# Kernel tuning notes

Hardware: AMD Instinct MI355X
Metric: run time of the kernel (lower is better)

## Reference

```python
import jax, jax.numpy as jnp
import numpy as np

EPS = 1e-5

def mesh_conv(x, gemm, w, b):
    # x: [B, C, E] edge features; gemm: [B, E, 4] int neighbor edge ids
    B, C, E = x.shape
    self_idx = jnp.broadcast_to(jnp.arange(E, dtype=gemm.dtype)[None, :, None], (B, E, 1))
    G = jnp.concatenate([self_idx, gemm], axis=2) + 1          # [B, E, 5], 0 = zero-pad slot
    xp = jnp.concatenate([jnp.zeros((B, C, 1), x.dtype), x], axis=2)  # [B, C, E+1]
    # f[b,c,e,k] = xp[b,c,G[b,e,k]]
    f = jax.vmap(lambda xb, gb: xb[:, gb])(xp, G)              # [B, C, E, 5]
    f0 = f[..., 0]
    x1 = f[..., 1] + f[..., 3]
    x2 = f[..., 2] + f[..., 4]
    x3 = jnp.abs(f[..., 1] - f[..., 3])
    x4 = jnp.abs(f[..., 2] - f[..., 4])
    Gm = jnp.stack([f0, x1, x2, x3, x4], axis=-1)              # [B, C, E, 5]
    # Conv2d kernel (1,5) over the 5 symmetric features
    out = jnp.einsum('bces,ocs->boe', Gm, w) + b[None, :, None]
    return out

def instance_norm(x):
    # InstanceNorm2d (affine=False): normalize per (b, c) over edge dim
    mean = jnp.mean(x, axis=2, keepdims=True)
    var = jnp.var(x, axis=2, keepdims=True)
    return (x - mean) * jax.lax.rsqrt(var + EPS)

def setup_inputs() -> dict:
    key = jax.random.key(0)
    ks = jax.random.split(key, 6)
    B, Cin, Cout, E = 2, 64, 128, 100000
    fe = jax.random.normal(ks[0], (B, Cin, E), dtype=jnp.float32)
    gemm = jax.random.randint(ks[1], (B, E, 4), 0, E, dtype=jnp.int32)
    w1 = jax.random.normal(ks[2], (Cout, Cin, 5), dtype=jnp.float32) * 0.05
    b1 = jax.random.normal(ks[3], (Cout,), dtype=jnp.float32) * 0.05
    w2 = jax.random.normal(ks[4], (Cout, Cout, 5), dtype=jnp.float32) * 0.05
    b2 = jax.random.normal(ks[5], (Cout,), dtype=jnp.float32) * 0.05
    return {"fe": fe, "gemm": gemm, "w1": w1, "b1": b1, "w2": w2, "b2": b2}

def reference(fe, gemm, w1, b1, w2, b2):
    x1 = jax.nn.relu(instance_norm(mesh_conv(fe, gemm, w1, b1)))
    x2 = instance_norm(mesh_conv(x1, gemm, w2, b2))
    x2 = jax.nn.relu(x2 + x1)
    return x2  # [B, Cout, E]; pool=0 so before_pool is None
```

## Files before the change

### kernel.cpp

```cpp
#include <hip/hip_runtime.h>
#include <hip/hip_bf16.h>

typedef unsigned short u16;
typedef __attribute__((ext_vector_type(4))) unsigned short u16x4;
typedef __attribute__((ext_vector_type(8))) unsigned short u16x8;
typedef __attribute__((ext_vector_type(8))) short s16x8;
typedef __attribute__((ext_vector_type(4))) float f32x4;

__device__ __forceinline__ float bf2f(u16 u){
  union { unsigned int i; float f; } v; v.i = ((unsigned int)u) << 16; return v.f;
}
__device__ __forceinline__ u16 f2bf(float f){
  union { float f; unsigned int i; } v; v.f = f;
  unsigned int r = v.i + 0x7fffu + ((v.i >> 16) & 1u);
  return (u16)(r >> 16);
}
__device__ __forceinline__ u16 f2bfh(float f){
  __hip_bfloat16 h = __float2bfloat16(f);
  return *reinterpret_cast<u16*>(&h);
}

__global__ __launch_bounds__(256) void prep_w(
    const float* __restrict__ src, u16* __restrict__ dst, int cout, int cin)
{
  const int n  = cout * cin * 5;
  const int KT = (cin * 5) / 32;
  const int i = blockIdx.x * 256 + threadIdx.x;
  if (i >= n) return;
  const int ii   = i & 7;
  const int lane = (i >> 3) & 63;
  const int kt   = (i >> 9) % KT;
  const int wv   = i / (KT * 512);
  const int o = wv * 16 + (lane & 15);
  const int k = kt * 32 + (lane >> 4) * 8 + ii;
  const int s = k / cin;
  const int c = k - s * cin;
  dst[i] = f2bf(src[(o * cin + c) * 5 + s]);
}

__global__ __launch_bounds__(256) void transpose64(
    const float* __restrict__ x, u16* __restrict__ xT, int E)
{
  __shared__ u16 tile[64][66];
  const int b   = blockIdx.z;
  const int e0  = blockIdx.x * 64;
  const int col = threadIdx.x & 63;
  const int r   = threadIdx.x >> 6;
  const int e   = e0 + col;
  #pragma unroll
  for (int k = 0; k < 16; k++) {
    const int c = r * 16 + k;
    float v = 0.f;
    if (e < E) v = x[((size_t)b * 64 + c) * (size_t)E + e];
    tile[c][col] = f2bf(v);
  }
  __syncthreads();
  const int e_l  = threadIdx.x >> 2;
  const int part = threadIdx.x & 3;
  const int eg   = e0 + e_l;
  if (eg < E) {
    u16* dst = xT + ((size_t)b * E + eg) * 64 + part * 16;
    #pragma unroll
    for (int h = 0; h < 2; h++) {
      u16x8 v;
      #pragma unroll
      for (int cc = 0; cc < 8; cc++) v[cc] = tile[part * 16 + h * 8 + cc][e_l];
      *(u16x8*)(dst + h * 8) = v;
    }
  }
}

__global__ __launch_bounds__(512, 6) void conv1_mfma(
    const u16* __restrict__ xT, const int* __restrict__ gidx,
    const u16* __restrict__ Wp, const float* __restrict__ bias,
    u16* __restrict__ y1b, float2* __restrict__ partials, int E, int nbx)
{
  constexpr int CIN = 64, EPB = 64, SUB = 8, KT = 10;
  constexpr int NT  = EPB / 16;
  __shared__ __align__(16) u16 F[5 * EPB * CIN];

  const int b  = blockIdx.z;
  const int bx = blockIdx.x;
  const int t  = threadIdx.x;
  const int e_l = t / SUB;
  const int sub = t % SUB;
  const int lane = t & 63, wv = t >> 6;
  const int lr = lane & 15, quad = lane >> 4;
  const size_t e_raw = (size_t)bx * EPB + e_l;
  const int e = (int)(e_raw < (size_t)E ? e_raw : (size_t)(E - 1));

  int rows[5];
  {
    const int4 g = *(const int4*)(gidx + ((size_t)b * E + e) * 4);
    rows[0] = e; rows[1] = g.x; rows[2] = g.y; rows[3] = g.z; rows[4] = g.w;
  }
  const u16* base = xT + (size_t)b * E * CIN + sub * 8;
  const u16* wbase = Wp + ((size_t)wv * KT * 64 + lane) * 8;

  u16x8 raw[5];
  #pragma unroll
  for (int j = 0; j < 5; j++)
    raw[j] = *(const u16x8*)(base + (size_t)rows[j] * CIN);
  __builtin_amdgcn_sched_barrier(0);

  {
    const int pc = (sub ^ (e_l & 7)) * 8;
    u16x8 o1, o2, o3, o4;
    #pragma unroll
    for (int c = 0; c < 8; c++) {
      const float a1 = bf2f(raw[1][c]), a2 = bf2f(raw[2][c]);
      const float a3 = bf2f(raw[3][c]), a4 = bf2f(raw[4][c]);
      o1[c] = f2bfh(a1 + a3);
      o2[c] = f2bfh(a2 + a4);
      o3[c] = f2bfh(fabsf(a1 - a3));
      o4[c] = f2bfh(fabsf(a2 - a4));
    }
    *(u16x8*)&F[(0 * EPB + e_l) * CIN + pc] = raw[0];
    *(u16x8*)&F[(1 * EPB + e_l) * CIN + pc] = o1;
    *(u16x8*)&F[(2 * EPB + e_l) * CIN + pc] = o2;
    *(u16x8*)&F[(3 * EPB + e_l) * CIN + pc] = o3;
    *(u16x8*)&F[(4 * EPB + e_l) * CIN + pc] = o4;
  }
  __syncthreads();

  f32x4 acc[NT];
  #pragma unroll
  for (int j = 0; j < NT; j++) acc[j] = (f32x4){0.f, 0.f, 0.f, 0.f};
  #pragma unroll
  for (int kt = 0; kt < KT; kt++) {
    const int s  = kt >> 1, cb = (kt & 1) * 32;
    const int chk = ((cb >> 3) + quad) ^ (lr & 7);
    const s16x8 a0 = *(const s16x8*)(wbase + kt * 512);
    #pragma unroll
    for (int j = 0; j < NT; j++) {
      const s16x8 bj = *(const s16x8*)&F[(s * EPB + j * 16 + lr) * CIN + chk * 8];
      acc[j] = __builtin_amdgcn_mfma_f32_16x16x32_bf16(bj, a0, acc[j], 0, 0, 0);
    }
  }

  const int ch = wv * 16 + lr;
  const float bv = bias[ch];
  float s = 0.f, s2 = 0.f;
  #pragma unroll
  for (int j = 0; j < NT; j++) {
    #pragma unroll
    for (int r = 0; r < 4; r++) {
      const int el = j * 16 + quad * 4 + r;
      const size_t eg = (size_t)bx * EPB + el;
      if (eg < (size_t)E) {
        const float v = acc[j][r] + bv;
        y1b[((size_t)b * E + eg) * 128 + ch] = f2bfh(v);
        s += v; s2 += v * v;
      }
    }
  }
  s  += __shfl_xor(s, 16);  s  += __shfl_xor(s, 32);
  s2 += __shfl_xor(s2, 16); s2 += __shfl_xor(s2, 32);
  if (lane < 16)
    partials[(size_t)(b * 128 + ch) * nbx + bx] = make_float2(s, s2);
}

__global__ __launch_bounds__(512, 6) void conv2_mfma(
    const u16* __restrict__ x1b, const int* __restrict__ gidx,
    const u16* __restrict__ Wp, const float* __restrict__ bias,
    const float2* __restrict__ stats1,
    u16* __restrict__ y2b, float2* __restrict__ partials, int E, int nbx)
{
  constexpr int CIN = 128, EPB = 32, SUB = 16, KT = 20;
  constexpr int NT  = EPB / 16;
  __shared__ __align__(16) u16 F[5 * EPB * CIN];

  const int b  = blockIdx.z;
  const int bx = blockIdx.x;
  const int t  = threadIdx.x;
  const int e_l = t / SUB;
  const int sub = t % SUB;
  const int lane = t & 63, wv = t >> 6;
  const int lr = lane & 15, quad = lane >> 4;
  const size_t e_raw = (size_t)bx * EPB + e_l;
  const int e = (int)(e_raw < (size_t)E ? e_raw : (size_t)(E - 1));

  int rows[5];
  {
    const int4 g = *(const int4*)(gidx + ((size_t)b * E + e) * 4);
    rows[0] = e; rows[1] = g.x; rows[2] = g.y; rows[3] = g.z; rows[4] = g.w;
  }
  const u16* base = x1b + (size_t)b * E * 128 + sub * 8;
  const u16* wbase = Wp + ((size_t)wv * KT * 64 + lane) * 8;

  u16x8 raw[5];
  #pragma unroll
  for (int j = 0; j < 5; j++)
    raw[j] = *(const u16x8*)(base + (size_t)rows[j] * 128);
  f32x4 st[4];
  {
    const float* sp = (const float*)(stats1 + b * 128 + sub * 8);
    #pragma unroll
    for (int q = 0; q < 4; q++) st[q] = *(const f32x4*)(sp + q * 4);
  }
  __builtin_amdgcn_sched_barrier(0);

  {
    const int pc = (sub ^ (e_l & 7)) * 8;
    u16x8 o0, o1, o2, o3, o4;
    #pragma unroll
    for (int c = 0; c < 8; c++) {
      const float nm = st[c >> 1][(c & 1) * 2];
      const float rr = st[c >> 1][(c & 1) * 2 + 1];
      float x[5];
      #pragma unroll
      for (int j = 0; j < 5; j++) {
        float v = fmaf(bf2f(raw[j][c]), rr, nm);
        x[j] = v < 0.f ? 0.f : v;
      }
      o0[c] = f2bfh(x[0]);
      o1[c] = f2bfh(x[1] + x[3]);
      o2[c] = f2bfh(x[2] + x[4]);
      o3[c] = f2bfh(fabsf(x[1] - x[3]));
      o4[c] = f2bfh(fabsf(x[2] - x[4]));
    }
    *(u16x8*)&F[(0 * EPB + e_l) * CIN + pc] = o0;
    *(u16x8*)&F[(1 * EPB + e_l) * CIN + pc] = o1;
    *(u16x8*)&F[(2 * EPB + e_l) * CIN + pc] = o2;
    *(u16x8*)&F[(3 * EPB + e_l) * CIN + pc] = o3;
    *(u16x8*)&F[(4 * EPB + e_l) * CIN + pc] = o4;
  }
  __syncthreads();

  f32x4 acc[NT];
  #pragma unroll
  for (int j = 0; j < NT; j++) acc[j] = (f32x4){0.f, 0.f, 0.f, 0.f};
  #pragma unroll
  for (int kt = 0; kt < KT; kt++) {
    const int s  = kt >> 2, cb = (kt & 3) * 32;
    const int chk = ((cb >> 3) + quad) ^ (lr & 7);
    const s16x8 a0 = *(const s16x8*)(wbase + kt * 512);
    #pragma unroll
    for (int j = 0; j < NT; j++) {
      const s16x8 bj = *(const s16x8*)&F[(s * EPB + j * 16 + lr) * CIN + chk * 8];
      acc[j] = __builtin_amdgcn_mfma_f32_16x16x32_bf16(a0, bj, acc[j], 0, 0, 0);
    }
  }

  const size_t ybase = (size_t)b * 128;
  const int m0 = wv * 16 + quad * 4;
  const float4 bs = *(const float4*)(bias + m0);
  #pragma unroll
  for (int r = 0; r < 4; r++) {
    const int m = m0 + r;
    const float bv = ((const float*)&bs)[r];
    float s = 0.f, s2 = 0.f;
    #pragma unroll
    for (int j = 0; j < NT; j++) {
      const size_t eg = (size_t)bx * EPB + j * 16 + lr;
      if (eg < (size_t)E) {
        const float v = acc[j][r] + bv;
        y2b[(ybase + m) * E + eg] = f2bfh(v);
        s += v; s2 += v * v;
      }
    }
    #pragma unroll
    for (int mk = 1; mk < 16; mk <<= 1) {
      s  += __shfl_xor(s,  mk);
      s2 += __shfl_xor(s2, mk);
    }
    if (lr == 0)
      partials[(size_t)(b * 128 + m) * nbx + bx] = make_float2(s, s2);
  }
}

__global__ __launch_bounds__(256) void stats_finalize(
    const float2* __restrict__ partials, float2* __restrict__ stats,
    int nbx, int E)
{
  const int row = blockIdx.x;
  const float2* p = partials + (size_t)row * nbx;
  float s = 0.f, s2 = 0.f;
  for (int i = threadIdx.x; i < nbx; i += 256) {
    const float2 v = p[i];
    s += v.x; s2 += v.y;
  }
  #pragma unroll
  for (int off = 32; off > 0; off >>= 1) {
    s  += __shfl_down(s, off);
    s2 += __shfl_down(s2, off);
  }
  __shared__ float rs[4], rs2[4];
  const int wv = threadIdx.x >> 6;
  if ((threadIdx.x & 63) == 0) { rs[wv] = s; rs2[wv] = s2; }
  __syncthreads();
  if (threadIdx.x == 0) {
    s  = rs[0] + rs[1] + rs[2] + rs[3];
    s2 = rs2[0] + rs2[1] + rs2[2] + rs2[3];
    const float mean = s / E;
    const float var  = s2 / E - mean * mean;
    const float rstd = rsqrtf(var + 1e-5f);
    stats[row] = make_float2(-mean * rstd, rstd);
  }
}

__global__ __launch_bounds__(256) void final_k(
    const u16* __restrict__ y2b, const u16* __restrict__ y1b,
    const float2* __restrict__ st1, const float2* __restrict__ st2,
    float* __restrict__ out, int E)
{
  __shared__ float tile[32][65];
  const int b  = blockIdx.z;
  const int o0 = blockIdx.y * 32;
  const int e0 = blockIdx.x * 64;
  const int t  = threadIdx.x;

  {
    const int e_l  = t >> 2;
    const int part = t & 3;
    const int eg   = e0 + e_l;
    if (eg < E) {
      const u16* src = y1b + ((size_t)b * E + eg) * 128 + o0 + part * 8;
      const u16x8 v = *(const u16x8*)src;
      #pragma unroll
      for (int i = 0; i < 8; i++) {
        const float2 s1 = st1[b * 128 + o0 + part * 8 + i];
        float x = fmaf(bf2f(v[i]), s1.y, s1.x);
        tile[part * 8 + i][e_l] = x < 0.f ? 0.f : x;
      }
    }
  }
  __syncthreads();

  {
    const int col = t & 63;
    const int r   = t >> 6;
    const int eg  = e0 + col;
    if (eg < E) {
      #pragma unroll
      for (int k = 0; k < 8; k++) {
        const int o = o0 + r * 8 + k;
        const float2 s2 = st2[b * 128 + o];
        const size_t idx = ((size_t)b * 128 + o) * E + eg;
        float v = fmaf(bf2f(y2b[idx]), s2.y, s2.x) + tile[r * 8 + k][col];
        v = v < 0.f ? 0.f : v;
        __builtin_nontemporal_store(v, out + idx);
      }
    }
  }
}

extern "C" void kernel_launch(void* const* d_in, const int* in_sizes, int n_in,
                              void* d_out, int out_size, void* d_ws, size_t ws_size,
                              hipStream_t stream)
{
  const float* fe  = (const float*)d_in[0];
  const int*   gmm = (const int*)d_in[1];
  const float* w1  = (const float*)d_in[2];
  const float* b1  = (const float*)d_in[3];
  const float* w2  = (const float*)d_in[4];
  const float* b2  = (const float*)d_in[5];
  float* out = (float*)d_out;

  const int B = 2, CIN = 64, COUT = 128;
  const int E = in_sizes[0] / (B * CIN);
  const int nbx1 = (E + 63) / 64;
  const int nbx2 = (E + 31) / 32;

  char* p = (char*)d_ws;
  auto alloc = [&](size_t bytes) -> char* {
    char* q = p; p += (bytes + 255) & ~(size_t)255; return q;
  };
  const size_t feT_b = (size_t)B * E * CIN * 2;
  const size_t y2_b  = (size_t)B * COUT * E * 2;
  char* regA = alloc(y2_b > feT_b ? y2_b : feT_b);
  u16*   feT = (u16*)regA;
  u16*   y2b = (u16*)regA;
  u16*   y1b = (u16*)alloc((size_t)B * E * COUT * 2);
  float2* stats1 = (float2*)alloc((size_t)B * COUT * sizeof(float2));
  float2* stats2 = (float2*)alloc((size_t)B * COUT * sizeof(float2));
  u16* w1b = (u16*)alloc((size_t)COUT * CIN * 5 * 2);
  u16* w2b = (u16*)alloc((size_t)COUT * COUT * 5 * 2);
  float2* partials = (float2*)d_out;

  const int n_w1 = COUT * CIN * 5, n_w2 = COUT * COUT * 5;
  prep_w <<<dim3((n_w1 + 255) / 256), 256, 0, stream>>>(w1, w1b, COUT, CIN);
  prep_w <<<dim3((n_w2 + 255) / 256), 256, 0, stream>>>(w2, w2b, COUT, COUT);

  transpose64 <<<dim3((E + 63) / 64, 1, B), 256, 0, stream>>>(fe, feT, E);
  conv1_mfma <<<dim3(nbx1, 1, B), 512, 0, stream>>>(feT, gmm, w1b, b1, y1b, partials, E, nbx1);
  stats_finalize <<<dim3(B * COUT), 256, 0, stream>>>(partials, stats1, nbx1, E);
  conv2_mfma <<<dim3(nbx2, 1, B), 512, 0, stream>>>(y1b, gmm, w2b, b2, stats1, y2b, partials, E, nbx2);
  stats_finalize <<<dim3(B * COUT), 256, 0, stream>>>(partials, stats2, nbx2, E);
  final_k <<<dim3((E + 63) / 64, COUT / 32, B), 256, 0, stream>>>(y2b, y1b, stats1, stats2, out, E);
}
```

Baseline: 329.9 us.

## Loop conv blocks over four tiles with register prefetch of next gather

Each conv1/conv2 block now processes four consecutive edge tiles in a loop instead of one. While the current tile's MFMA runs, the next tile's neighbour indices and rows are gathered into registers. The goal is to hide the random-gather latency behind compute and to amortise weight/bias setup across tiles. In exchange the grid is four times smaller, which may reduce parallelism and occupancy-based latency hiding, and each tile adds an extra barrier.

New measurement: 448.2 us. 35.9% more time.

```diff
diff --git a/kernel.cpp b/kernel.cpp
--- a/kernel.cpp
+++ b/kernel.cpp
@@ -75,89 +75,111 @@
     const u16* __restrict__ Wp, const float* __restrict__ bias,
     u16* __restrict__ y1b, float2* __restrict__ partials, int E, int nbx)
 {
-  constexpr int CIN = 64, EPB = 64, SUB = 8, KT = 10;
+  constexpr int CIN = 64, EPB = 64, SUB = 8, KT = 10, NTL = 4;
   constexpr int NT  = EPB / 16;
   __shared__ __align__(16) u16 F[5 * EPB * CIN];
 
   const int b  = blockIdx.z;
-  const int bx = blockIdx.x;
   const int t  = threadIdx.x;
   const int e_l = t / SUB;
   const int sub = t % SUB;
   const int lane = t & 63, wv = t >> 6;
   const int lr = lane & 15, quad = lane >> 4;
-  const size_t e_raw = (size_t)bx * EPB + e_l;
-  const int e = (int)(e_raw < (size_t)E ? e_raw : (size_t)(E - 1));
-
-  int rows[5];
-  {
-    const int4 g = *(const int4*)(gidx + ((size_t)b * E + e) * 4);
-    rows[0] = e; rows[1] = g.x; rows[2] = g.y; rows[3] = g.z; rows[4] = g.w;
-  }
-  const u16* base = xT + (size_t)b * E * CIN + sub * 8;
+  const int tbeg = blockIdx.x * NTL;
+
+  const u16* base  = xT + (size_t)b * E * CIN + sub * 8;
   const u16* wbase = Wp + ((size_t)wv * KT * 64 + lane) * 8;
-
-  u16x8 raw[5];
-  #pragma unroll
-  for (int j = 0; j < 5; j++)
-    raw[j] = *(const u16x8*)(base + (size_t)rows[j] * CIN);
-  __builtin_amdgcn_sched_barrier(0);
-
-  {
-    const int pc = (sub ^ (e_l & 7)) * 8;
-    u16x8 o1, o2, o3, o4;
-    #pragma unroll
-    for (int c = 0; c < 8; c++) {
-      const float a1 = bf2f(raw[1][c]), a2 = bf2f(raw[2][c]);
-      const float a3 = bf2f(raw[3][c]), a4 = bf2f(raw[4][c]);
-      o1[c] = f2bfh(a1 + a3);
-      o2[c] = f2bfh(a2 + a4);
-      o3[c] = f2bfh(fabsf(a1 - a3));
-      o4[c] = f2bfh(fabsf(a2 - a4));
-    }
-    *(u16x8*)&F[(0 * EPB + e_l) * CIN + pc] = raw[0];
-    *(u16x8*)&F[(1 * EPB + e_l) * CIN + pc] = o1;
-    *(u16x8*)&F[(2 * EPB + e_l) * CIN + pc] = o2;
-    *(u16x8*)&F[(3 * EPB + e_l) * CIN + pc] = o3;
-    *(u16x8*)&F[(4 * EPB + e_l) * CIN + pc] = o4;
-  }
-  __syncthreads();
-
-  f32x4 acc[NT];
-  #pragma unroll
-  for (int j = 0; j < NT; j++) acc[j] = (f32x4){0.f, 0.f, 0.f, 0.f};
-  #pragma unroll
-  for (int kt = 0; kt < KT; kt++) {
-    const int s  = kt >> 1, cb = (kt & 1) * 32;
-    const int chk = ((cb >> 3) + quad) ^ (lr & 7);
-    const s16x8 a0 = *(const s16x8*)(wbase + kt * 512);
-    #pragma unroll
-    for (int j = 0; j < NT; j++) {
-      const s16x8 bj = *(const s16x8*)&F[(s * EPB + j * 16 + lr) * CIN + chk * 8];
-      acc[j] = __builtin_amdgcn_mfma_f32_16x16x32_bf16(bj, a0, acc[j], 0, 0, 0);
-    }
-  }
-
   const int ch = wv * 16 + lr;
   const float bv = bias[ch];
-  float s = 0.f, s2 = 0.f;
-  #pragma unroll
-  for (int j = 0; j < NT; j++) {
-    #pragma unroll
-    for (int r = 0; r < 4; r++) {
-      const int el = j * 16 + quad * 4 + r;
-      const size_t eg = (size_t)bx * EPB + el;
-      if (eg < (size_t)E) {
-        const float v = acc[j][r] + bv;
-        y1b[((size_t)b * E + eg) * 128 + ch] = f2bfh(v);
-        s += v; s2 += v * v;
-      }
-    }
-  }
-  s  += __shfl_xor(s, 16);  s  += __shfl_xor(s, 32);
-  s2 += __shfl_xor(s2, 16); s2 += __shfl_xor(s2, 32);
-  if (lane < 16)
-    partials[(size_t)(b * 128 + ch) * nbx + bx] = make_float2(s, s2);
+  const int pc = (sub ^ (e_l & 7)) * 8;
+
+  u16x8 raw[5];
+  {
+    int er = tbeg * EPB + e_l;
+    const int e = er < E ? er : E - 1;
+    const int4 g = *(const int4*)(gidx + ((size_t)b * E + e) * 4);
+    int rows[5] = {e, g.x, g.y, g.z, g.w};
+    #pragma unroll
+    for (int j = 0; j < 5; j++)
+      raw[j] = *(const u16x8*)(base + (size_t)rows[j] * CIN);
+  }
+  __builtin_amdgcn_sched_barrier(0);
+
+  for (int it = 0; it < NTL; ++it) {
+    const int tcur = tbeg + it;
+    const bool hasNext = (it + 1 < NTL);
+
+    int4 gn; int en = 0;
+    if (hasNext) {
+      int er = (tcur + 1) * EPB + e_l;
+      en = er < E ? er : E - 1;
+      gn = *(const int4*)(gidx + ((size_t)b * E + en) * 4);
+    }
+
+    {
+      u16x8 o1, o2, o3, o4;
+      #pragma unroll
+      for (int c = 0; c < 8; c++) {
+        const float a1 = bf2f(raw[1][c]), a2 = bf2f(raw[2][c]);
+        const float a3 = bf2f(raw[3][c]), a4 = bf2f(raw[4][c]);
+        o1[c] = f2bfh(a1 + a3);
+        o2[c] = f2bfh(a2 + a4);
+        o3[c] = f2bfh(fabsf(a1 - a3));
+        o4[c] = f2bfh(fabsf(a2 - a4));
+      }
+      *(u16x8*)&F[(0 * EPB + e_l) * CIN + pc] = raw[0];
+      *(u16x8*)&F[(1 * EPB + e_l) * CIN + pc] = o1;
+      *(u16x8*)&F[(2 * EPB + e_l) * CIN + pc] = o2;
+      *(u16x8*)&F[(3 * EPB + e_l) * CIN + pc] = o3;
+      *(u16x8*)&F[(4 * EPB + e_l) * CIN + pc] = o4;
+    }
+    __syncthreads();
+
+    if (hasNext) {
+      int rows[5] = {en, gn.x, gn.y, gn.z, gn.w};
+      #pragma unroll
+      for (int j = 0; j < 5; j++)
+        raw[j] = *(const u16x8*)(base + (size_t)rows[j] * CIN);
+      __builtin_amdgcn_sched_barrier(0);
+    }
+
+    f32x4 acc[NT];
+    #pragma unroll
+    for (int j = 0; j < NT; j++) acc[j] = (f32x4){0.f, 0.f, 0.f, 0.f};
+    #pragma unroll
+    for (int kt = 0; kt < KT; kt++) {
+      const int s  = kt >> 1, cb = (kt & 1) * 32;
+      const int chk = ((cb >> 3) + quad) ^ (lr & 7);
+      const s16x8 a0 = *(const s16x8*)(wbase + kt * 512);
+      #pragma unroll
+      for (int j = 0; j < NT; j++) {
+        const s16x8 bj = *(const s16x8*)&F[(s * EPB + j * 16 + lr) * CIN + chk * 8];
+        acc[j] = __builtin_amdgcn_mfma_f32_16x16x32_bf16(bj, a0, acc[j], 0, 0, 0);
+      }
+    }
+
+    if (tcur < nbx) {
+      float s = 0.f, s2 = 0.f;
+      #pragma unroll
+      for (int j = 0; j < NT; j++) {
+        #pragma unroll
+        for (int r = 0; r < 4; r++) {
+          const int el = j * 16 + quad * 4 + r;
+          const size_t eg = (size_t)tcur * EPB + el;
+          if (eg < (size_t)E) {
+            const float v = acc[j][r] + bv;
+            y1b[((size_t)b * E + eg) * 128 + ch] = f2bfh(v);
+            s += v; s2 += v * v;
+          }
+        }
+      }
+      s  += __shfl_xor(s, 16);  s  += __shfl_xor(s, 32);
+      s2 += __shfl_xor(s2, 16); s2 += __shfl_xor(s2, 32);
+      if (lane < 16)
+        partials[(size_t)(b * 128 + ch) * nbx + tcur] = make_float2(s, s2);
+    }
+    __syncthreads();
+  }
 }
 
 __global__ __launch_bounds__(512, 6) void conv2_mfma(
@@ -166,106 +188,129 @@
     const float2* __restrict__ stats1,
     u16* __restrict__ y2b, float2* __restrict__ partials, int E, int nbx)
 {
-  constexpr int CIN = 128, EPB = 32, SUB = 16, KT = 20;
+  constexpr int CIN = 128, EPB = 32, SUB = 16, KT = 20, NTL = 4;
   constexpr int NT  = EPB / 16;
   __shared__ __align__(16) u16 F[5 * EPB * CIN];
 
   const int b  = blockIdx.z;
-  const int bx = blockIdx.x;
   const int t  = threadIdx.x;
   const int e_l = t / SUB;
   const int sub = t % SUB;
   const int lane = t & 63, wv = t >> 6;
   const int lr = lane & 15, quad = lane >> 4;
-  const size_t e_raw = (size_t)bx * EPB + e_l;
-  const int e = (int)(e_raw < (size_t)E ? e_raw : (size_t)(E - 1));
-
-  int rows[5];
-  {
-    const int4 g = *(const int4*)(gidx + ((size_t)b * E + e) * 4);
-    rows[0] = e; rows[1] = g.x; rows[2] = g.y; rows[3] = g.z; rows[4] = g.w;
-  }
-  const u16* base = x1b + (size_t)b * E * 128 + sub * 8;
+  const int tbeg = blockIdx.x * NTL;
+
+  const u16* base  = x1b + (size_t)b * E * 128 + sub * 8;
   const u16* wbase = Wp + ((size_t)wv * KT * 64 + lane) * 8;
-
-  u16x8 raw[5];
-  #pragma unroll
-  for (int j = 0; j < 5; j++)
-    raw[j] = *(const u16x8*)(base + (size_t)rows[j] * 128);
+  const int pc = (sub ^ (e_l & 7)) * 8;
+
   f32x4 st[4];
   {
     const float* sp = (const float*)(stats1 + b * 128 + sub * 8);
     #pragma unroll
     for (int q = 0; q < 4; q++) st[q] = *(const f32x4*)(sp + q * 4);
   }
-  __builtin_amdgcn_sched_barrier(0);
-
-  {
-    const int pc = (sub ^ (e_l & 7)) * 8;
-    u16x8 o0, o1, o2, o3, o4;
-    #pragma unroll
-    for (int c = 0; c < 8; c++) {
-      const float nm = st[c >> 1][(c & 1) * 2];
-      const float rr = st[c >> 1][(c & 1) * 2 + 1];
-      float x[5];
-      #pragma unroll
-      for (int j = 0; j < 5; j++) {
-        float v = fmaf(bf2f(raw[j][c]), rr, nm);
-        x[j] = v < 0.f ? 0.f : v;
-      }
-      o0[c] = f2bfh(x[0]);
-      o1[c] = f2bfh(x[1] + x[3]);
-      o2[c] = f2bfh(x[2] + x[4]);
-      o3[c] = f2bfh(fabsf(x[1] - x[3]));
-      o4[c] = f2bfh(fabsf(x[2] - x[4]));
-    }
-    *(u16x8*)&F[(0 * EPB + e_l) * CIN + pc] = o0;
-    *(u16x8*)&F[(1 * EPB + e_l) * CIN + pc] = o1;
-    *(u16x8*)&F[(2 * EPB + e_l) * CIN + pc] = o2;
-    *(u16x8*)&F[(3 * EPB + e_l) * CIN + pc] = o3;
-    *(u16x8*)&F[(4 * EPB + e_l) * CIN + pc] = o4;
-  }
-  __syncthreads();
-
-  f32x4 acc[NT];
-  #pragma unroll
-  for (int j = 0; j < NT; j++) acc[j] = (f32x4){0.f, 0.f, 0.f, 0.f};
-  #pragma unroll
-  for (int kt = 0; kt < KT; kt++) {
-    const int s  = kt >> 2, cb = (kt & 3) * 32;
-    const int chk = ((cb >> 3) + quad) ^ (lr & 7);
-    const s16x8 a0 = *(const s16x8*)(wbase + kt * 512);
-    #pragma unroll
-    for (int j = 0; j < NT; j++) {
-      const s16x8 bj = *(const s16x8*)&F[(s * EPB + j * 16 + lr) * CIN + chk * 8];
-      acc[j] = __builtin_amdgcn_mfma_f32_16x16x32_bf16(a0, bj, acc[j], 0, 0, 0);
-    }
-  }
-
-  const size_t ybase = (size_t)b * 128;
   const int m0 = wv * 16 + quad * 4;
   const float4 bs = *(const float4*)(bias + m0);
-  #pragma unroll
-  for (int r = 0; r < 4; r++) {
-    const int m = m0 + r;
-    const float bv = ((const float*)&bs)[r];
-    float s = 0.f, s2 = 0.f;
-    #pragma unroll
-    for (int j = 0; j < NT; j++) {
-      const size_t eg = (size_t)bx * EPB + j * 16 + lr;
-      if (eg < (size_t)E) {
-        const float v = acc[j][r] + bv;
-        y2b[(ybase + m) * E + eg] = f2bfh(v);
-        s += v; s2 += v * v;
-      }
-    }
-    #pragma unroll
-    for (int mk = 1; mk < 16; mk <<= 1) {
-      s  += __shfl_xor(s,  mk);
-      s2 += __shfl_xor(s2, mk);
-    }
-    if (lr == 0)
-      partials[(size_t)(b * 128 + m) * nbx + bx] = make_float2(s, s2);
+
+  u16x8 raw[5];
+  {
+    int er = tbeg * EPB + e_l;
+    const int e = er < E ? er : E - 1;
+    const int4 g = *(const int4*)(gidx + ((size_t)b * E + e) * 4);
+    int rows[5] = {e, g.x, g.y, g.z, g.w};
+    #pragma unroll
+    for (int j = 0; j < 5; j++)
+      raw[j] = *(const u16x8*)(base + (size_t)rows[j] * 128);
+  }
+  __builtin_amdgcn_sched_barrier(0);
+
+  for (int it = 0; it < NTL; ++it) {
+    const int tcur = tbeg + it;
+    const bool hasNext = (it + 1 < NTL);
+
+    int4 gn; int en = 0;
+    if (hasNext) {
+      int er = (tcur + 1) * EPB + e_l;
+      en = er < E ? er : E - 1;
+      gn = *(const int4*)(gidx + ((size_t)b * E + en) * 4);
+    }
+
+    {
+      u16x8 o0, o1, o2, o3, o4;
+      #pragma unroll
+      for (int c = 0; c < 8; c++) {
+        const float nm = st[c >> 1][(c & 1) * 2];
+        const float rr = st[c >> 1][(c & 1) * 2 + 1];
+        float x[5];
+        #pragma unroll
+        for (int j = 0; j < 5; j++) {
+          float v = fmaf(bf2f(raw[j][c]), rr, nm);
+          x[j] = v < 0.f ? 0.f : v;
+        }
+        o0[c] = f2bfh(x[0]);
+        o1[c] = f2bfh(x[1] + x[3]);
+        o2[c] = f2bfh(x[2] + x[4]);
+        o3[c] = f2bfh(fabsf(x[1] - x[3]));
+        o4[c] = f2bfh(fabsf(x[2] - x[4]));
+      }
+      *(u16x8*)&F[(0 * EPB + e_l) * CIN + pc] = o0;
+      *(u16x8*)&F[(1 * EPB + e_l) * CIN + pc] = o1;
+      *(u16x8*)&F[(2 * EPB + e_l) * CIN + pc] = o2;
+      *(u16x8*)&F[(3 * EPB + e_l) * CIN + pc] = o3;
+      *(u16x8*)&F[(4 * EPB + e_l) * CIN + pc] = o4;
+    }
+    __syncthreads();
+
+    if (hasNext) {
+      int rows[5] = {en, gn.x, gn.y, gn.z, gn.w};
+      #pragma unroll
+      for (int j = 0; j < 5; j++)
+        raw[j] = *(const u16x8*)(base + (size_t)rows[j] * 128);
+      __builtin_amdgcn_sched_barrier(0);
+    }
+
+    f32x4 acc[NT];
+    #pragma unroll
+    for (int j = 0; j < NT; j++) acc[j] = (f32x4){0.f, 0.f, 0.f, 0.f};
+    #pragma unroll
+    for (int kt = 0; kt < KT; kt++) {
+      const int s  = kt >> 2, cb = (kt & 3) * 32;
+      const int chk = ((cb >> 3) + quad) ^ (lr & 7);
+      const s16x8 a0 = *(const s16x8*)(wbase + kt * 512);
+      #pragma unroll
+      for (int j = 0; j < NT; j++) {
+        const s16x8 bj = *(const s16x8*)&F[(s * EPB + j * 16 + lr) * CIN + chk * 8];
+        acc[j] = __builtin_amdgcn_mfma_f32_16x16x32_bf16(a0, bj, acc[j], 0, 0, 0);
+      }
+    }
+
+    if (tcur < nbx) {
+      const size_t ybase = (size_t)b * 128;
+      #pragma unroll
+      for (int r = 0; r < 4; r++) {
+        const int m = m0 + r;
+        const float bvv = ((const float*)&bs)[r];
+        float s = 0.f, s2 = 0.f;
+        #pragma unroll
+        for (int j = 0; j < NT; j++) {
+          const size_t eg = (size_t)tcur * EPB + j * 16 + lr;
+          if (eg < (size_t)E) {
+            const float v = acc[j][r] + bvv;
+            y2b[(ybase + m) * E + eg] = f2bfh(v);
+            s += v; s2 += v * v;
+          }
+        }
+        #pragma unroll
+        for (int mk = 1; mk < 16; mk <<= 1) {
+          s  += __shfl_xor(s,  mk);
+          s2 += __shfl_xor(s2, mk);
+        }
+        if (lr == 0)
+          partials[(size_t)(b * 128 + m) * nbx + tcur] = make_float2(s, s2);
+      }
+    }
+    __syncthreads();
   }
 }
 
@@ -361,6 +406,8 @@
   const int E = in_sizes[0] / (B * CIN);
   const int nbx1 = (E + 63) / 64;
   const int nbx2 = (E + 31) / 32;
+  const int gb1  = (nbx1 + 3) / 4;
+  const int gb2  = (nbx2 + 3) / 4;
 
   char* p = (char*)d_ws;
   auto alloc = [&](size_t bytes) -> char* {
@@ -383,9 +430,9 @@
   prep_w <<<dim3((n_w2 + 255) / 256), 256, 0, stream>>>(w2, w2b, COUT, COUT);
 
   transpose64 <<<dim3((E + 63) / 64, 1, B), 256, 0, stream>>>(fe, feT, E);
-  conv1_mfma <<<dim3(nbx1, 1, B), 512, 0, stream>>>(feT, gmm, w1b, b1, y1b, partials, E, nbx1);
+  conv1_mfma <<<dim3(gb1, 1, B), 512, 0, stream>>>(feT, gmm, w1b, b1, y1b, partials, E, nbx1);
   stats_finalize <<<dim3(B * COUT), 256, 0, stream>>>(partials, stats1, nbx1, E);
-  conv2_mfma <<<dim3(nbx2, 1, B), 512, 0, stream>>>(y1b, gmm, w2b, b2, stats1, y2b, partials, E, nbx2);
+  conv2_mfma <<<dim3(gb2, 1, B), 512, 0, stream>>>(y1b, gmm, w2b, b2, stats1, y2b, partials, E, nbx2);
   stats_finalize <<<dim3(B * COUT), 256, 0, stream>>>(partials, stats2, nbx2, E);
   final_k <<<dim3((E + 63) / 64, COUT / 32, B), 256, 0, stream>>>(y2b, y1b, stats1, stats2, out, E);
 }
```
